# Performance work log

Measured on AMD Instinct MI355X. Metric: run time of the kernel, lower is better.

The kernel has to match this reference:

```python
import jax, jax.numpy as jnp
import numpy as np

N = 50000        # nodes
E = 400000       # edges (avg degree 8)
T = 4            # edge types
D_IN = 64        # input feature dim
D_OUT = 128      # GGNN hidden / output dim
B = 64           # graphs in batch
STEPS = 8        # GRU propagation steps


def setup_inputs() -> dict:
    key = jax.random.key(0)
    ks = jax.random.split(key, 10)
    s = 1.0 / np.sqrt(D_OUT)
    features = jax.random.normal(ks[0], (N, D_IN), jnp.float32)
    src = jax.random.randint(ks[1], (E,), 0, N, jnp.int32)
    dst = jax.random.randint(ks[2], (E,), 0, N, jnp.int32)
    etype = jax.random.randint(ks[3], (E,), 0, T, jnp.int32)
    node2graph = jnp.sort(jax.random.randint(ks[4], (N,), 0, B, jnp.int32))
    # per-edge-type message Linear(out, out)
    W_msg = jax.random.normal(ks[5], (T, D_OUT, D_OUT), jnp.float32) * s
    b_msg = jnp.zeros((T, D_OUT), jnp.float32)
    # GRUCell(out, out): gate order (r, z, n) as in torch
    w_ih = jax.random.normal(ks[6], (D_OUT, 3 * D_OUT), jnp.float32) * s
    b_ih = jnp.zeros((3 * D_OUT,), jnp.float32)
    w_hh = jax.random.normal(ks[7], (D_OUT, 3 * D_OUT), jnp.float32) * s
    b_hh = jnp.zeros((3 * D_OUT,), jnp.float32)
    # classifier Linear(out, 2)
    W_cls = jax.random.normal(ks[8], (D_OUT, 2), jnp.float32) * s
    b_cls = jnp.zeros((2,), jnp.float32)
    return {"features": features, "src": src, "dst": dst, "etype": etype,
            "node2graph": node2graph, "W_msg": W_msg, "b_msg": b_msg,
            "w_ih": w_ih, "b_ih": b_ih, "w_hh": w_hh, "b_hh": b_hh,
            "W_cls": W_cls, "b_cls": b_cls}


def reference(features, src, dst, etype, node2graph, W_msg, b_msg,
              w_ih, b_ih, w_hh, b_hh, W_cls, b_cls):
    n = features.shape[0]
    # zero-pad input features to D_OUT (as in GGNN.forward)
    h1 = jnp.concatenate(
        [features, jnp.zeros((n, D_OUT - D_IN), features.dtype)], axis=-1)

    def step(h, _):
        # transform every node by every etype weight: [N, T, D]
        t = jnp.einsum('nd,tde->nte', h, W_msg) + b_msg
        msgs = t[src, etype]                       # [E, D] gather per edge
        a = jax.ops.segment_sum(msgs, dst, num_segments=n)  # scatter-sum
        # torch GRUCell(a, h), gates ordered (r, z, n)
        gi = a @ w_ih + b_ih
        gh = h @ w_hh + b_hh
        i_r, i_z, i_n = jnp.split(gi, 3, axis=-1)
        h_r, h_z, h_n = jnp.split(gh, 3, axis=-1)
        r = jax.nn.sigmoid(i_r + h_r)
        z = jax.nn.sigmoid(i_z + h_z)
        ng = jnp.tanh(i_n + r * h_n)
        return (1.0 - z) * ng + z * h, None

    h, _ = jax.lax.scan(step, h1, None, length=STEPS)
    hres = h + h1                                   # residual as in forward
    # read_out == 'sum': per-graph segment sum (dgl.sum_nodes)
    feats_g = jax.ops.segment_sum(hres, node2graph, num_segments=B)  # [B, D]
    return feats_g @ W_cls + b_cls                  # [B, 2]
```

## Files before the change

### kernel.cpp

```cpp
#include <hip/hip_runtime.h>
#include <hip/hip_bf16.h>
#include <math.h>

#define NN 50000
#define EE 400000
#define TT 4
#define DIN 64
#define DD 128
#define BB 64
#define STEPS 8
#define KAGG 544
#define NGATES 512
#define NBIN (4 * NN)
#define NBLK ((NBIN + 255) / 256)
#define MT64 ((NN + 63) / 64)
#define W2F_N (21 * 12288)

typedef __attribute__((ext_vector_type(8))) short bf16x8;
typedef __attribute__((ext_vector_type(4))) float f32x4;
typedef __attribute__((address_space(3))) void lds_void;
typedef __attribute__((address_space(1))) void glob_void;

__device__ inline float bf2f(__hip_bfloat16 x) { return __bfloat162float(x); }

__device__ inline float s2f(short s) {
    unsigned int u = ((unsigned int)(unsigned short)s) << 16;
    float f;
    __builtin_memcpy(&f, &u, 4);
    return f;
}

__global__ void k_init_h(const float* __restrict__ feat, float* __restrict__ h1,
                         __hip_bfloat16* __restrict__ hb) {
    int idx = blockIdx.x * blockDim.x + threadIdx.x;
    if (idx >= NN * DD) return;
    int v = idx >> 7, d = idx & 127;
    float val = (d < DIN) ? feat[v * DIN + d] : 0.0f;
    h1[idx] = val;
    hb[idx] = __float2bfloat16(val);
}

__global__ void k_zero_i32(int* __restrict__ p, int n) {
    int idx = blockIdx.x * blockDim.x + threadIdx.x;
    if (idx < n) p[idx] = 0;
}
__global__ void k_zero_f32(float* __restrict__ p, int n) {
    int idx = blockIdx.x * blockDim.x + threadIdx.x;
    if (idx < n) p[idx] = 0.0f;
}

__global__ void k_hist(const int* __restrict__ dst, const int* __restrict__ etype,
                       int* __restrict__ deg2) {
    int e = blockIdx.x * blockDim.x + threadIdx.x;
    if (e < EE) atomicAdd(&deg2[dst[e] * 4 + etype[e]], 1);
}

__global__ __launch_bounds__(256) void k_scan_bsum(const int* __restrict__ deg2,
                                                   int* __restrict__ bsum) {
    __shared__ int red[256];
    int tid = threadIdx.x;
    int i = blockIdx.x * 256 + tid;
    int v = (i < NBIN) ? deg2[i] : 0;
    red[tid] = v;
    __syncthreads();
#pragma unroll
    for (int s = 128; s > 0; s >>= 1) {
        if (tid < s) red[tid] += red[tid + s];
        __syncthreads();
    }
    if (tid == 0) bsum[blockIdx.x] = red[0];
}

__global__ __launch_bounds__(1024) void k_scan_boff(const int* __restrict__ bsum,
                                                    int* __restrict__ boff) {
    __shared__ int s[1024];
    int tid = threadIdx.x;
    int v = (tid < NBLK) ? bsum[tid] : 0;
    s[tid] = v;
    __syncthreads();
    for (int d = 1; d < 1024; d <<= 1) {
        int t = (tid >= d) ? s[tid - d] : 0;
        __syncthreads();
        s[tid] += t;
        __syncthreads();
    }
    if (tid < NBLK) boff[tid] = s[tid] - v;
}

__global__ __launch_bounds__(256) void k_scan_final(const int* __restrict__ deg2,
                                                    const int* __restrict__ boff,
                                                    int* __restrict__ off2,
                                                    int* __restrict__ cursor) {
    __shared__ int s[256];
    int tid = threadIdx.x;
    int i = blockIdx.x * 256 + tid;
    int v = (i < NBIN) ? deg2[i] : 0;
    s[tid] = v;
    __syncthreads();
#pragma unroll
    for (int d = 1; d < 256; d <<= 1) {
        int t = (tid >= d) ? s[tid - d] : 0;
        __syncthreads();
        s[tid] += t;
        __syncthreads();
    }
    int excl = boff[blockIdx.x] + s[tid] - v;
    if (i < NBIN) {
        off2[i] = excl;
        cursor[i] = excl;
        if (i == NBIN - 1) off2[NBIN] = excl + v;
    }
}

__global__ void k_fill(const int* __restrict__ dst, const int* __restrict__ src,
                       const int* __restrict__ etype, int* __restrict__ cursor,
                       int* __restrict__ csr_src) {
    int e = blockIdx.x * blockDim.x + threadIdx.x;
    if (e < EE) {
        int pos = atomicAdd(&cursor[dst[e] * 4 + etype[e]], 1);
        csr_src[pos] = src[e];
    }
}

__global__ void k_counts(const int* __restrict__ off2, __hip_bfloat16* __restrict__ g) {
    int idx = blockIdx.x * blockDim.x + threadIdx.x;
    if (idx >= NN * 16) return;
    int v = idx >> 4, j = idx & 15;
    float x = 0.0f, y = 0.0f;
    if (j < 2) {
        int t0 = 2 * j;
        x = (float)(off2[4 * v + t0 + 1] - off2[4 * v + t0]);
        y = (float)(off2[4 * v + t0 + 2] - off2[4 * v + t0 + 1]);
    }
    __hip_bfloat162 o;
    o.x = __float2bfloat16(x);
    o.y = __float2bfloat16(y);
    ((__hip_bfloat162*)(g + (size_t)v * KAGG))[256 + j] = o;
}

__global__ void k_prep_w2f(const float* __restrict__ Wm, const float* __restrict__ bm,
                           const float* __restrict__ wih, const float* __restrict__ whh,
                           const float* __restrict__ bih, const float* __restrict__ bhh,
                           __hip_bfloat16* __restrict__ W2f, float* __restrict__ bias512) {
    int idx = blockIdx.x * blockDim.x + threadIdx.x;
    if (idx < W2F_N) {
        int kc = idx / 12288;
        int r1 = idx % 12288;
        int gb = r1 >> 12;
        int r2 = r1 & 4095;
        int w = r2 >> 9;
        int r3 = r2 & 511;
        int l = r3 >> 3;
        int j = r3 & 7;
        int npart = w * 16 + (l & 15);
        int kin = ((l >> 4) << 3) + j;
        float v = 0.0f;
        if (kc < 17) {
            int k = kc * 32 + kin;
            int n = gb * 128 + npart;
            if (k < 512) {
                int t = k >> 7, kd = k & 127;
                const float* wr = Wm + (t << 14) + (kd << 7);
                float s = 0.0f;
#pragma unroll 4
                for (int e = 0; e < 128; ++e) s += wr[e] * wih[e * 384 + n];
                v = s;
            } else if (k < 516) {
                const float* br = bm + ((k - 512) << 7);
                float s = 0.0f;
#pragma unroll 4
                for (int e = 0; e < 128; ++e) s += br[e] * wih[e * 384 + n];
                v = s;
            }
        } else {
            int kh = (kc - 17) * 32 + kin;
            int nlog = (gb < 2) ? gb * 128 + npart : 384 + npart;
            int col = (nlog < 256) ? nlog : nlog - 128;
            v = whh[kh * 384 + col];
        }
        W2f[idx] = __float2bfloat16(v);
        return;
    }
    int b = idx - W2F_N;
    if (b < NGATES) {
        float v;
        if (b < 256) v = bih[b] + bhh[b];
        else if (b < 384) v = bih[b];
        else v = bhh[b - 128];
        bias512[b] = v;
    }
}

__global__ __launch_bounds__(256) void k_agg(const __hip_bfloat16* __restrict__ hb,
                                             const int* __restrict__ off2,
                                             const int* __restrict__ csr_src,
                                             __hip_bfloat16* __restrict__ g) {
    const int node = (blockIdx.x * blockDim.x + threadIdx.x) >> 6;
    const int lane = threadIdx.x & 63;
    if (node >= NN) return;
    const int t = lane >> 4;
    const int sub = lane & 15;
    const int p0 = off2[4 * node + t];
    const int p1 = off2[4 * node + t + 1];
    float a[8];
#pragma unroll
    for (int j = 0; j < 8; ++j) a[j] = 0.0f;
    int p = p0;
    for (; p + 1 < p1; p += 2) {
        int s0 = csr_src[p];
        int s1 = csr_src[p + 1];
        bf16x8 v0 = *(const bf16x8*)(hb + (size_t)s0 * DD + sub * 8);
        bf16x8 v1 = *(const bf16x8*)(hb + (size_t)s1 * DD + sub * 8);
#pragma unroll
        for (int j = 0; j < 8; ++j) a[j] += s2f(v0[j]) + s2f(v1[j]);
    }
    if (p < p1) {
        int s0 = csr_src[p];
        bf16x8 v0 = *(const bf16x8*)(hb + (size_t)s0 * DD + sub * 8);
#pragma unroll
        for (int j = 0; j < 8; ++j) a[j] += s2f(v0[j]);
    }
    bf16x8 o;
#pragma unroll
    for (int j = 0; j < 8; ++j) {
        __hip_bfloat16 b = __float2bfloat16(a[j]);
        o[j] = *(short*)&b;
    }
    *(bf16x8*)(g + (size_t)node * KAGG + t * 128 + sub * 8) = o;
}

__global__ __launch_bounds__(512, 4) void k_step(const __hip_bfloat16* __restrict__ g,
                                                 const __hip_bfloat16* __restrict__ W2f,
                                                 const float* __restrict__ bias512,
                                                 const __hip_bfloat16* __restrict__ hbi,
                                                 __hip_bfloat16* __restrict__ hbo) {
    __shared__ __align__(16) short As[4][64 * 32];
    __shared__ __align__(16) short Bs[2][12288];
    const int tid = threadIdx.x;
    const int lane = tid & 63;
    const int wave = tid >> 6;
    const int row0 = blockIdx.x * 64;
    const int quad = lane >> 4;
    const int m16 = lane & 15;
    const int koff = ((quad ^ ((m16 ^ (m16 >> 2)) & 3)) << 3);
    const int bfbase = (wave * 64 + lane) * 8;

    const int arow = tid >> 2;
    const int apart = (tid & 3) ^ ((arow ^ (arow >> 2)) & 3);
    int agrow = row0 + arow;
    if (agrow >= NN) agrow = NN - 1;
    const __hip_bfloat16* gA = g + (size_t)agrow * KAGG + apart * 8;
    const __hip_bfloat16* hA = hbi + (size_t)agrow * DD + apart * 8;
    const __hip_bfloat16* bsrc = W2f + tid * 8;

    auto stage_A = [&](int kc) {
        if (wave < 4) {
            const glob_void* srcA = (kc < 17)
                                        ? (const glob_void*)(gA + kc * 32)
                                        : (const glob_void*)(hA + (kc - 17) * 32);
            __builtin_amdgcn_global_load_lds(srcA, (lds_void*)&As[kc & 3][(wave * 64) * 8],
                                             16, 0, 0);
        }
    };
    auto stage_B = [&](int kc) {
        const __hip_bfloat16* s0 = bsrc + kc * 12288;
#pragma unroll
        for (int i = 0; i < 3; ++i) {
            __builtin_amdgcn_global_load_lds((const glob_void*)(s0 + i * 4096),
                                             (lds_void*)&Bs[kc & 1][(wave * 64 + i * 512) * 8],
                                             16, 0, 0);
        }
    };

    f32x4 acc[4][4];
#pragma unroll
    for (int rt = 0; rt < 4; ++rt)
#pragma unroll
        for (int c = 0; c < 4; ++c) acc[rt][c] = (f32x4){0.f, 0.f, 0.f, 0.f};

    stage_B(0);
    stage_A(0);
    stage_A(1);
    stage_A(2);

    for (int ki = 0; ki < 21; ++ki) {
        if (wave < 4) {
            if (ki == 0)
                asm volatile("s_waitcnt vmcnt(2)" ::: "memory");
            else if (ki <= 18)
                asm volatile("s_waitcnt vmcnt(1)" ::: "memory");
            else
                asm volatile("s_waitcnt vmcnt(0)" ::: "memory");
        } else {
            asm volatile("s_waitcnt vmcnt(0)" ::: "memory");
        }
        __builtin_amdgcn_s_barrier();
        asm volatile("" ::: "memory");
        __builtin_amdgcn_sched_barrier(0);

        if (ki + 1 < 21) stage_B(ki + 1);
        if (ki + 3 < 21) stage_A(ki + 3);

        bf16x8 af[4];
#pragma unroll
        for (int rt = 0; rt < 4; ++rt)
            af[rt] = *(const bf16x8*)&As[ki & 3][(rt * 16 + m16) * 32 + koff];
        bf16x8 b0 = *(const bf16x8*)&Bs[ki & 1][bfbase];
        bf16x8 b1 = *(const bf16x8*)&Bs[ki & 1][bfbase + 4096];
        bf16x8 b2 = *(const bf16x8*)&Bs[ki & 1][bfbase + 8192];
#pragma unroll
        for (int rt = 0; rt < 4; ++rt)
            acc[rt][0] = __builtin_amdgcn_mfma_f32_16x16x32_bf16(af[rt], b0, acc[rt][0], 0, 0, 0);
#pragma unroll
        for (int rt = 0; rt < 4; ++rt)
            acc[rt][1] = __builtin_amdgcn_mfma_f32_16x16x32_bf16(af[rt], b1, acc[rt][1], 0, 0, 0);
        if (ki < 17) {
#pragma unroll
            for (int rt = 0; rt < 4; ++rt)
                acc[rt][2] = __builtin_amdgcn_mfma_f32_16x16x32_bf16(af[rt], b2, acc[rt][2], 0, 0, 0);
        } else {
#pragma unroll
            for (int rt = 0; rt < 4; ++rt)
                acc[rt][3] = __builtin_amdgcn_mfma_f32_16x16x32_bf16(af[rt], b2, acc[rt][3], 0, 0, 0);
        }
    }
    __syncthreads();

    short* Ht = &Bs[0][0];
    {
        const int d = wave * 16 + m16;
        const float brs = bias512[d];
        const float bzs = bias512[128 + d];
        const float bin_ = bias512[256 + d];
        const float bhn = bias512[384 + d];
#pragma unroll
        for (int rt = 0; rt < 4; ++rt) {
#pragma unroll
            for (int j = 0; j < 4; ++j) {
                const int rowl = rt * 16 + quad * 4 + j;
                const int grow = row0 + rowl;
                const float rs = acc[rt][0][j] + brs;
                const float zs = acc[rt][1][j] + bzs;
                const float inn = acc[rt][2][j] + bin_;
                const float hnn = acc[rt][3][j] + bhn;
                const float rr = 1.0f / (1.0f + __expf(-rs));
                const float zz = 1.0f / (1.0f + __expf(-zs));
                const float ex = __expf(2.0f * (inn + rr * hnn));
                const float ng = 1.0f - 2.0f / (ex + 1.0f);
                const float hv =
                    bf2f(hbi[(size_t)(grow < NN ? grow : NN - 1) * DD + d]);
                const float o = (1.0f - zz) * ng + zz * hv;
                __hip_bfloat16 ob = __float2bfloat16(o);
                Ht[rowl * 128 + d] = *(short*)&ob;
            }
        }
    }
    __syncthreads();
    {
        const int row = tid >> 3;
        const int col = (tid & 7) * 16;
        if (row0 + row < NN) {
            bf16x8 v0 = *(const bf16x8*)&Ht[row * 128 + col];
            bf16x8 v1 = *(const bf16x8*)&Ht[row * 128 + col + 8];
            __hip_bfloat16* dstp = hbo + (size_t)(row0 + row) * DD + col;
            *(bf16x8*)dstp = v0;
            *(bf16x8*)(dstp + 8) = v1;
        }
    }
}

__global__ __launch_bounds__(128) void k_readout(const __hip_bfloat16* __restrict__ h,
                                                 const float* __restrict__ h1,
                                                 const int* __restrict__ n2g,
                                                 float* __restrict__ feats) {
    const int CHN = 64;
    int d = threadIdx.x;
    int v0 = blockIdx.x * CHN;
    if (v0 >= NN) return;
    int v1 = v0 + CHN;
    if (v1 > NN) v1 = NN;
    float sum = 0.0f;
    int cur = n2g[v0];
    for (int v = v0; v < v1; ++v) {
        int gph = n2g[v];
        if (gph != cur) {
            atomicAdd(&feats[cur * DD + d], sum);
            sum = 0.0f;
            cur = gph;
        }
        sum += bf2f(h[(size_t)v * DD + d]) + h1[(size_t)v * DD + d];
    }
    atomicAdd(&feats[cur * DD + d], sum);
}

__global__ void k_cls(const float* __restrict__ feats, const float* __restrict__ Wc,
                      const float* __restrict__ bc, float* __restrict__ out) {
    int t = threadIdx.x;
    if (t >= BB * 2) return;
    int b = t >> 1, c = t & 1;
    float s = bc[c];
    for (int d = 0; d < DD; ++d) s += feats[b * DD + d] * Wc[d * 2 + c];
    out[t] = s;
}

extern "C" void kernel_launch(void* const* d_in, const int* in_sizes, int n_in, void* d_out,
                              int out_size, void* d_ws, size_t ws_size, hipStream_t stream) {
    const float* features = (const float*)d_in[0];
    const int* src = (const int*)d_in[1];
    const int* dst = (const int*)d_in[2];
    const int* etype = (const int*)d_in[3];
    const int* n2g = (const int*)d_in[4];
    const float* W_msg = (const float*)d_in[5];
    const float* b_msg = (const float*)d_in[6];
    const float* w_ih = (const float*)d_in[7];
    const float* b_ih = (const float*)d_in[8];
    const float* w_hh = (const float*)d_in[9];
    const float* b_hh = (const float*)d_in[10];
    const float* W_cls = (const float*)d_in[11];
    const float* b_cls = (const float*)d_in[12];
    float* out = (float*)d_out;

    char* ws = (char*)d_ws;
    size_t o = 0;
    auto alloc = [&](size_t bytes) {
        o = (o + 255) & ~(size_t)255;
        void* p = ws + o;
        o += bytes;
        return p;
    };
    int* deg2 = (int*)alloc(sizeof(int) * NBIN);
    int* off2 = (int*)alloc(sizeof(int) * (NBIN + 1));
    int* cursor = (int*)alloc(sizeof(int) * NBIN);
    int* bsum = (int*)alloc(sizeof(int) * NBLK);
    int* boff = (int*)alloc(sizeof(int) * NBLK);
    int* csr_src = (int*)alloc(sizeof(int) * EE);
    __hip_bfloat16* W2f = (__hip_bfloat16*)alloc(sizeof(__hip_bfloat16) * W2F_N);
    float* bias512 = (float*)alloc(sizeof(float) * NGATES);
    float* hini = (float*)alloc(sizeof(float) * (size_t)NN * DD);
    __hip_bfloat16* hbfA = (__hip_bfloat16*)alloc(sizeof(__hip_bfloat16) * (size_t)NN * DD);
    __hip_bfloat16* hbfB = (__hip_bfloat16*)alloc(sizeof(__hip_bfloat16) * (size_t)NN * DD);
    __hip_bfloat16* g = (__hip_bfloat16*)alloc(sizeof(__hip_bfloat16) * (size_t)NN * KAGG);
    float* feats = (float*)alloc(sizeof(float) * BB * DD);

    k_init_h<<<(NN * DD + 255) / 256, 256, 0, stream>>>(features, hini, hbfA);
    k_zero_i32<<<(NBIN + 255) / 256, 256, 0, stream>>>(deg2, NBIN);
    k_zero_f32<<<(BB * DD + 255) / 256, 256, 0, stream>>>(feats, BB * DD);
    k_hist<<<(EE + 255) / 256, 256, 0, stream>>>(dst, etype, deg2);
    k_scan_bsum<<<NBLK, 256, 0, stream>>>(deg2, bsum);
    k_scan_boff<<<1, 1024, 0, stream>>>(bsum, boff);
    k_scan_final<<<NBLK, 256, 0, stream>>>(deg2, boff, off2, cursor);
    k_fill<<<(EE + 255) / 256, 256, 0, stream>>>(dst, src, etype, cursor, csr_src);
    k_counts<<<(NN * 16 + 255) / 256, 256, 0, stream>>>(off2, g);
    {
        int prep_n = W2F_N + NGATES;
        k_prep_w2f<<<(prep_n + 255) / 256, 256, 0, stream>>>(W_msg, b_msg, w_ih, w_hh,
                                                             b_ih, b_hh, W2f, bias512);
    }

    __hip_bfloat16* hbc = hbfA;
    __hip_bfloat16* hbx = hbfB;
    for (int s = 0; s < STEPS; ++s) {
        k_agg<<<(NN * 64 + 255) / 256, 256, 0, stream>>>(hbc, off2, csr_src, g);
        k_step<<<MT64, 512, 0, stream>>>(g, W2f, bias512, hbc, hbx);
        __hip_bfloat16* tb = hbc; hbc = hbx; hbx = tb;
    }
    k_readout<<<(NN + 63) / 64, 128, 0, stream>>>(hbc, hini, n2g, feats);
    k_cls<<<1, 128, 0, stream>>>(feats, W_cls, b_cls, out);
}
```

Baseline: 782.6 us.

## Load GRU weight fragments directly from global memory instead of staging through LDS

```diff
diff --git a/kernel.cpp b/kernel.cpp
--- a/kernel.cpp
+++ b/kernel.cpp
@@ -234,8 +234,8 @@
                                                  const float* __restrict__ bias512,
                                                  const __hip_bfloat16* __restrict__ hbi,
                                                  __hip_bfloat16* __restrict__ hbo) {
-    __shared__ __align__(16) short As[4][64 * 32];
-    __shared__ __align__(16) short Bs[2][12288];
+    __shared__ __align__(16) short As[2][64 * 32];
+    __shared__ __align__(16) short Ht[64 * 132];
     const int tid = threadIdx.x;
     const int lane = tid & 63;
     const int wave = tid >> 6;
@@ -243,7 +243,6 @@
     const int quad = lane >> 4;
     const int m16 = lane & 15;
     const int koff = ((quad ^ ((m16 ^ (m16 >> 2)) & 3)) << 3);
-    const int bfbase = (wave * 64 + lane) * 8;
 
     const int arow = tid >> 2;
     const int apart = (tid & 3) ^ ((arow ^ (arow >> 2)) & 3);
@@ -251,26 +250,17 @@
     if (agrow >= NN) agrow = NN - 1;
     const __hip_bfloat16* gA = g + (size_t)agrow * KAGG + apart * 8;
     const __hip_bfloat16* hA = hbi + (size_t)agrow * DD + apart * 8;
-    const __hip_bfloat16* bsrc = W2f + tid * 8;
+    const __hip_bfloat16* bw = W2f + ((size_t)(wave * 64 + lane)) * 8;
 
     auto stage_A = [&](int kc) {
         if (wave < 4) {
             const glob_void* srcA = (kc < 17)
                                         ? (const glob_void*)(gA + kc * 32)
                                         : (const glob_void*)(hA + (kc - 17) * 32);
-            __builtin_amdgcn_global_load_lds(srcA, (lds_void*)&As[kc & 3][(wave * 64) * 8],
+            __builtin_amdgcn_global_load_lds(srcA, (lds_void*)&As[kc & 1][(wave * 64) * 8],
                                              16, 0, 0);
         }
     };
-    auto stage_B = [&](int kc) {
-        const __hip_bfloat16* s0 = bsrc + kc * 12288;
-#pragma unroll
-        for (int i = 0; i < 3; ++i) {
-            __builtin_amdgcn_global_load_lds((const glob_void*)(s0 + i * 4096),
-                                             (lds_void*)&Bs[kc & 1][(wave * 64 + i * 512) * 8],
-                                             16, 0, 0);
-        }
-    };
 
     f32x4 acc[4][4];
 #pragma unroll
@@ -278,36 +268,21 @@
 #pragma unroll
         for (int c = 0; c < 4; ++c) acc[rt][c] = (f32x4){0.f, 0.f, 0.f, 0.f};
 
-    stage_B(0);
     stage_A(0);
-    stage_A(1);
-    stage_A(2);
+    __syncthreads();
 
     for (int ki = 0; ki < 21; ++ki) {
-        if (wave < 4) {
-            if (ki == 0)
-                asm volatile("s_waitcnt vmcnt(2)" ::: "memory");
-            else if (ki <= 18)
-                asm volatile("s_waitcnt vmcnt(1)" ::: "memory");
-            else
-                asm volatile("s_waitcnt vmcnt(0)" ::: "memory");
-        } else {
-            asm volatile("s_waitcnt vmcnt(0)" ::: "memory");
-        }
-        __builtin_amdgcn_s_barrier();
-        asm volatile("" ::: "memory");
-        __builtin_amdgcn_sched_barrier(0);
-
-        if (ki + 1 < 21) stage_B(ki + 1);
-        if (ki + 3 < 21) stage_A(ki + 3);
+        if (ki + 1 < 21) stage_A(ki + 1);
+
+        const __hip_bfloat16* bp = bw + ki * 12288;
+        bf16x8 b0 = *(const bf16x8*)(bp);
+        bf16x8 b1 = *(const bf16x8*)(bp + 4096);
+        bf16x8 b2 = *(const bf16x8*)(bp + 8192);
 
         bf16x8 af[4];
 #pragma unroll
         for (int rt = 0; rt < 4; ++rt)
-            af[rt] = *(const bf16x8*)&As[ki & 3][(rt * 16 + m16) * 32 + koff];
-        bf16x8 b0 = *(const bf16x8*)&Bs[ki & 1][bfbase];
-        bf16x8 b1 = *(const bf16x8*)&Bs[ki & 1][bfbase + 4096];
-        bf16x8 b2 = *(const bf16x8*)&Bs[ki & 1][bfbase + 8192];
+            af[rt] = *(const bf16x8*)&As[ki & 1][(rt * 16 + m16) * 32 + koff];
 #pragma unroll
         for (int rt = 0; rt < 4; ++rt)
             acc[rt][0] = __builtin_amdgcn_mfma_f32_16x16x32_bf16(af[rt], b0, acc[rt][0], 0, 0, 0);
@@ -323,10 +298,9 @@
             for (int rt = 0; rt < 4; ++rt)
                 acc[rt][3] = __builtin_amdgcn_mfma_f32_16x16x32_bf16(af[rt], b2, acc[rt][3], 0, 0, 0);
         }
-    }
-    __syncthreads();
-
-    short* Ht = &Bs[0][0];
+        __syncthreads();
+    }
+
     {
         const int d = wave * 16 + m16;
         const float brs = bias512[d];
@@ -351,7 +325,7 @@
                     bf2f(hbi[(size_t)(grow < NN ? grow : NN - 1) * DD + d]);
                 const float o = (1.0f - zz) * ng + zz * hv;
                 __hip_bfloat16 ob = __float2bfloat16(o);
-                Ht[rowl * 128 + d] = *(short*)&ob;
+                Ht[rowl * 132 + d] = *(short*)&ob;
             }
         }
     }
@@ -360,8 +334,8 @@
         const int row = tid >> 3;
         const int col = (tid & 7) * 16;
         if (row0 + row < NN) {
-            bf16x8 v0 = *(const bf16x8*)&Ht[row * 128 + col];
-            bf16x8 v1 = *(const bf16x8*)&Ht[row * 128 + col + 8];
+            bf16x8 v0 = *(const bf16x8*)&Ht[row * 132 + col];
+            bf16x8 v1 = *(const bf16x8*)&Ht[row * 132 + col + 8];
             __hip_bfloat16* dstp = hbo + (size_t)(row0 + row) * DD + col;
             *(bf16x8*)dstp = v0;
             *(bf16x8*)(dstp + 8) = v1;
```

After: 753.3 us. 1.04x faster.
